# Kernel tuning notes

Hardware: AMD Instinct MI355X
Metric: run time of the kernel (lower is better)

The kernel has to match this reference:

```python
import jax, jax.numpy as jnp
import numpy as np

N_NODES = 50000


def gcn_conv(x, W, b, row, col, n):
    """PyG GCNConv with default add_self_loops=True, normalize=True.
    out[i] = sum_{e: col[e]=i} d^-1/2[row[e]] d^-1/2[i] * (x@W)[row[e]]
             + d^-1[i]*(x@W)[i] + b,  where d = in-degree + 1 (self-loop).
    """
    x_lin = x @ W                                   # [n, out_ch]
    ones = jnp.ones(row.shape[0], dtype=x.dtype)
    deg = jax.ops.segment_sum(ones, col, num_segments=n) + 1.0  # self-loop
    dinv = jax.lax.rsqrt(deg)                       # deg >= 1, safe
    norm = dinv[row] * dinv[col]                    # [E]
    msg = norm[:, None] * x_lin[row]                # [E, out_ch]
    agg = jax.ops.segment_sum(msg, col, num_segments=n)
    self_term = (dinv * dinv)[:, None] * x_lin      # self-loop contribution
    return agg + self_term + b


def setup_inputs() -> dict:
    key = jax.random.key(0)
    ks = jax.random.split(key, 10)
    in_ch, hid, out_ch = 128, 256, 64
    E = 800000
    x = jax.random.normal(ks[0], (N_NODES, in_ch), dtype=jnp.float32)
    edge_attr = jax.random.normal(ks[1], (E, 8), dtype=jnp.float32)  # unused by forward
    edge_index = jax.random.randint(ks[2], (2, E), 0, N_NODES, dtype=jnp.int64)
    def glorot(k, fan_in, fan_out):
        s = float(np.sqrt(6.0 / (fan_in + fan_out)))
        return jax.random.uniform(k, (fan_in, fan_out), jnp.float32, -s, s)
    return {
        "x": x,
        "edge_attr": edge_attr,
        "edge_index": edge_index,
        "W1": glorot(ks[3], in_ch, hid), "b1": jnp.zeros((hid,), jnp.float32),
        "W2": glorot(ks[4], hid, hid),  "b2": jnp.zeros((hid,), jnp.float32),
        "W3": glorot(ks[5], hid, out_ch), "b3": jnp.zeros((out_ch,), jnp.float32),
    }


def reference(x, edge_attr, edge_index, W1, b1, W2, b2, W3, b3):
    n = x.shape[0]
    row, col = edge_index[0], edge_index[1]
    h = jax.nn.sigmoid(gcn_conv(x, W1, b1, row, col, n))
    h = jax.nn.sigmoid(gcn_conv(h, W2, b2, row, col, n))
    # dropout(p=0.1) in eval mode is identity
    return gcn_conv(h, W3, b3, row, col, n)
```

## Files before the change

kernel.cpp:

```cpp
#include <hip/hip_runtime.h>
#include <hip/hip_bf16.h>

typedef __bf16 bf16x8_t __attribute__((ext_vector_type(8)));
typedef float f32x4_t __attribute__((ext_vector_type(4)));
typedef float f32x2_t __attribute__((ext_vector_type(2)));

__device__ __forceinline__ float bits2f(unsigned int u) {
    union { unsigned int u; float f; } c; c.u = u; return c.f;
}
__device__ __forceinline__ unsigned short f2bf_bits(float f) {
    __hip_bfloat16 h = __float2bfloat16(f);
    return __builtin_bit_cast(unsigned short, h);
}
__device__ __forceinline__ f32x2_t unpack_bf2(unsigned int u) {
    return (f32x2_t){bits2f(u << 16), bits2f(u & 0xffff0000u)};
}

__global__ void sentinel_fill(float* __restrict__ out, int n) {
    int i = blockIdx.x * blockDim.x + threadIdx.x;
    if (i < n) out[i] = 100.0f;
}

__global__ void init_combo(const unsigned int* __restrict__ ei, int* __restrict__ flags,
                           int* __restrict__ cnt, int M) {
    if (blockIdx.x == 0) {
        if (threadIdx.x < 64) {
            int lane = threadIdx.x;
            int cz = 0;
            #pragma unroll
            for (int j = 0; j < 4; ++j) {
                int idx = lane * 4 + j;
                cz += (ei[2 * idx + 1] == 0u);
            }
            #pragma unroll
            for (int off = 32; off; off >>= 1) cz += __shfl_down(cz, off);
            if (lane == 0) flags[0] = (cz > 200);
        }
    } else {
        int i = (blockIdx.x - 1) * 256 + threadIdx.x;
        if (i < M) cnt[i] = 0;
    }
}


__global__ void count_rank_dual2(const int* __restrict__ ei, int* __restrict__ cnt,
                                 int* __restrict__ rank, int* __restrict__ c32,
                                 int* __restrict__ r32, int E, int M,
                                 const int* __restrict__ flags) {
    int e = blockIdx.x * blockDim.x + threadIdx.x;
    if (e < E) {
        int r, c;
        if (flags[0]) { r = ei[2 * e]; c = ei[2 * E + 2 * e]; }
        else          { r = ei[e];     c = ei[E + e]; }
        c32[e] = c;
        r32[e] = r;
        int rk = 0;
        if ((unsigned)c < (unsigned)M) rk = atomicAdd(&cnt[c], 1);
        rank[e] = rk;
    }
}

__global__ void scan_blocks(const int* __restrict__ cnt, int* __restrict__ excl,
                            int* __restrict__ bsum, int n) {
    int tid = threadIdx.x;
    int i = blockIdx.x * 256 + tid;
    int lane = tid & 63, wv = tid >> 6;
    __shared__ int ws[4];
    int v = (i < n) ? cnt[i] : 0;
    int s = v;
    #pragma unroll
    for (int off = 1; off < 64; off <<= 1) {
        int t = __shfl_up(s, off);
        if (lane >= off) s += t;
    }
    if (lane == 63) ws[wv] = s;
    __syncthreads();
    if (tid == 0) { int a = 0; for (int q = 0; q < 4; ++q) { int t = ws[q]; ws[q] = a; a += t; } }
    __syncthreads();
    int ex = s - v + ws[wv];
    if (i < n) excl[i] = ex;
    if (tid == 255) bsum[blockIdx.x] = ex + v;
}

__global__ void scan_bsums(const int* __restrict__ bsum, int* __restrict__ boff,
                           int nb, int* __restrict__ colptr, int n) {
    int tid = threadIdx.x, lane = tid & 63, wv = tid >> 6;
    __shared__ int ws[4];
    __shared__ int carry;
    if (tid == 0) carry = 0;
    __syncthreads();
    for (int base = 0; base < nb; base += 256) {
        int i = base + tid;
        int v = (i < nb) ? bsum[i] : 0;
        int s = v;
        #pragma unroll
        for (int off = 1; off < 64; off <<= 1) {
            int t = __shfl_up(s, off);
            if (lane >= off) s += t;
        }
        if (lane == 63) ws[wv] = s;
        __syncthreads();
        if (tid == 0) { int a = carry; for (int q = 0; q < 4; ++q) { int t = ws[q]; ws[q] = a; a += t; } carry = a; }
        __syncthreads();
        int ex = s - v + ws[wv];
        if (i < nb) boff[i] = ex;
        __syncthreads();
    }
    if (tid == 0) colptr[n] = carry;
}

__global__ void scan_add_dinv(const int* __restrict__ excl, const int* __restrict__ boff,
                              const int* __restrict__ cnt, int* __restrict__ colptr,
                              float* __restrict__ dinv, int n) {
    int i = blockIdx.x * 256 + threadIdx.x;
    if (i < n) {
        colptr[i] = excl[i] + boff[blockIdx.x];
        dinv[i] = rsqrtf((float)cnt[i] + 1.0f);
    }
}

__global__ void fill_csr_part2(const int* __restrict__ c32, const int* __restrict__ r32,
                               const int* __restrict__ colptr, const int* __restrict__ rank,
                               int* __restrict__ esrc, int E, int M, int psz) {
    int part = blockIdx.x & 7;
    int e = (blockIdx.x >> 3) * 256 + threadIdx.x;
    int lo = part * psz;
    int hi = lo + psz; if (hi > M) hi = M;
    if (e < E) {
        int c = c32[e];
        if (c >= lo && c < hi) {
            int r = r32[e];
            if ((unsigned)r < (unsigned)M) {
                int p = colptr[c] + rank[e];
                if ((unsigned)p < (unsigned)E) esrc[p] = r;
            }
        }
    }
}

__global__ void prep_fused(const float* __restrict__ x, const float* __restrict__ dinv,
                           unsigned char* __restrict__ xs8,
                           const float* __restrict__ W1, const float* __restrict__ W2,
                           const float* __restrict__ W3,
                           unsigned short* __restrict__ Wt1, unsigned short* __restrict__ Wt2,
                           unsigned short* __restrict__ Wt3,
                           int M, int nps) {
    if ((int)blockIdx.x < nps) {
        int i = blockIdx.x * 256 + threadIdx.x;
        if (i < M * 32) {
            int row = i >> 5;
            float dv = dinv[row];
            float4 v = *(const float4*)(x + (size_t)i * 4);
            unsigned u = __builtin_amdgcn_cvt_pk_fp8_f32(v.x * dv, v.y * dv, 0, false);
            u = __builtin_amdgcn_cvt_pk_fp8_f32(v.z * dv, v.w * dv, u, true);
            *(unsigned*)(xs8 + (size_t)i * 4) = u;
        }
    } else {
        int i = ((int)blockIdx.x - nps) * 256 + threadIdx.x;
        if (i < 32768) {
            int k = i >> 8, n = i & 255;
            Wt1[n * 128 + k] = f2bf_bits(W1[i]);
        } else if (i < 32768 + 65536) {
            int j = i - 32768;
            int k = j >> 8, n = j & 255;
            Wt2[n * 256 + k] = f2bf_bits(W2[j]);
        } else if (i < 114688) {
            int j = i - 98304;
            int k = j >> 6, n = j & 63;
            Wt3[n * 256 + k] = f2bf_bits(W3[j]);
        }
    }
}

template<int K, int BN, int NTOT, int EPI>
__global__ __launch_bounds__(256) void gemm_tile(
    const __bf16* __restrict__ A,
    const unsigned short* __restrict__ Bt,
    const float* __restrict__ dinv,
    const float* __restrict__ bias,
    void* __restrict__ Y,
    int M)
{
    constexpr int KS = (K > 128) ? 128 : K;
    constexpr int KP = KS + 8;
    constexpr int NT = BN / 2 / 16;
    __shared__ unsigned short Bs[BN * KP];

    const int tid  = threadIdx.x;
    const int lane = tid & 63;
    const int wave = tid >> 6;
    const int wm   = wave >> 1;
    const int wn   = wave & 1;
    const int quad = lane >> 4;
    const int l16  = lane & 15;
    const int n0   = blockIdx.y * BN;

    int mrow[4];
#pragma unroll
    for (int mt = 0; mt < 4; ++mt) {
        int r = blockIdx.x * 128 + wm * 64 + mt * 16 + l16;
        mrow[mt] = (r < M) ? r : (M - 1);
    }

    f32x4_t acc[4][NT];
#pragma unroll
    for (int mt = 0; mt < 4; ++mt)
#pragma unroll
        for (int t = 0; t < NT; ++t) acc[mt][t] = (f32x4_t){0.f, 0.f, 0.f, 0.f};

    const unsigned short* BsW = &Bs[(wn * (BN / 2)) * KP];

    for (int kh = 0; kh < K; kh += KS) {
        constexpr int CH = BN * KS / 8;
        for (int idx = tid; idx < CH; idx += 256) {
            int n  = idx / (KS / 8);
            int k8 = idx - n * (KS / 8);
            uint4 v = *(const uint4*)(Bt + (size_t)(n0 + n) * K + kh + k8 * 8);
            *(uint4*)&Bs[n * KP + k8 * 8] = v;
        }
        __syncthreads();

#pragma unroll
        for (int kc = 0; kc < KS; kc += 32) {
            bf16x8_t a[4], b[NT];
#pragma unroll
            for (int mt = 0; mt < 4; ++mt)
                a[mt] = *(const bf16x8_t*)(A + (size_t)mrow[mt] * K + kh + kc + quad * 8);
#pragma unroll
            for (int t = 0; t < NT; ++t)
                b[t] = *(const bf16x8_t*)&BsW[(t * 16 + l16) * KP + kc + quad * 8];
#pragma unroll
            for (int mt = 0; mt < 4; ++mt)
#pragma unroll
                for (int t = 0; t < NT; ++t)
                    acc[mt][t] = __builtin_amdgcn_mfma_f32_16x16x32_bf16(a[mt], b[t], acc[mt][t], 0, 0, 0);
        }
        if (kh + KS < K) __syncthreads();
    }

    float bv[NT];
    if constexpr (EPI == 1) {
#pragma unroll
        for (int t = 0; t < NT; ++t)
            bv[t] = bias[n0 + wn * (BN / 2) + t * 16 + l16];
    }

#pragma unroll
    for (int mt = 0; mt < 4; ++mt) {
        int rowbase = blockIdx.x * 128 + wm * 64 + mt * 16 + quad * 4;
#pragma unroll
        for (int r = 0; r < 4; ++r) {
            int rrow = rowbase + r;
            if (rrow < M) {
                if constexpr (EPI == 0) {
                    float dv = dinv[rrow];
#pragma unroll
                    for (int t = 0; t < NT; ++t) {
                        int ccol = n0 + wn * (BN / 2) + t * 16 + l16;
                        ((__hip_bfloat16*)Y)[(size_t)rrow * NTOT + ccol] =
                            __float2bfloat16(acc[mt][t][r] * dv);
                    }
                } else if constexpr (EPI == 1) {
#pragma unroll
                    for (int t = 0; t < NT; ++t) {
                        int ccol = n0 + wn * (BN / 2) + t * 16 + l16;
                        float o = acc[mt][t][r] + bv[t];
                        o = 1.f / (1.f + __expf(-o));
                        ((__hip_bfloat16*)Y)[(size_t)rrow * NTOT + ccol] = __float2bfloat16(o);
                    }
                } else {
                    float dv = dinv[rrow];
#pragma unroll
                    for (int t = 0; t < NT; ++t) {
                        int ccol = n0 + wn * (BN / 2) + t * 16 + l16;
                        float o = acc[mt][t][r] * dv;
                        int pk = __builtin_amdgcn_cvt_pk_fp8_f32(o, o, 0, false);
                        ((unsigned char*)Y)[(size_t)rrow * NTOT + ccol] = (unsigned char)(pk & 0xff);
                    }
                }
            }
        }
    }
}

__global__ __launch_bounds__(256) void aggregate_fp8_v4(
    const unsigned char* __restrict__ Y8,
    const int* __restrict__ colptr,
    const int* __restrict__ esrc,
    const float* __restrict__ dinv,
    const float* __restrict__ bias,
    unsigned short* __restrict__ H,
    int M, int Etot)
{
    const int lane = threadIdx.x & 63;
    const int wave = threadIdx.x >> 6;
    int node = blockIdx.x * 4 + wave;
    if (node >= M) return;

    int s = colptr[node];
    int e = colptr[node + 1];
    if (s < 0) s = 0;
    if (e > Etot) e = Etot;
    if (e < s) e = s;
    int n = e - s;

    const char* Yb = (const char*)Y8;
    const unsigned lb = (unsigned)(lane * 4);

    unsigned su = *(const unsigned*)(Yb + (((unsigned)node) << 8) + lb);

    f32x2_t a0 = {0.f, 0.f}, a1 = {0.f, 0.f};

    auto gather8 = [&](unsigned* u, int base) {
        #pragma unroll
        for (int k = 0; k < 8; ++k) {
            unsigned off = (((unsigned)esrc[s + base + k]) << 8) + lb;
            u[k] = *(const unsigned*)(Yb + off);
        }
    };
    auto acc8 = [&](const unsigned* u) {
        #pragma unroll
        for (int k = 0; k < 8; ++k) {
            a0 += __builtin_amdgcn_cvt_pk_f32_fp8(u[k], false);
            a1 += __builtin_amdgcn_cvt_pk_f32_fp8(u[k], true);
        }
    };

    unsigned ua[8], ub[8];
    int NB = n >> 3;
    if (NB > 0) {
        gather8(ua, 0);
        int i = 1;
        for (; i + 1 < NB; i += 2) {
            gather8(ub, i << 3);
            acc8(ua);
            gather8(ua, (i + 1) << 3);
            acc8(ub);
        }
        if (i < NB) {
            gather8(ub, i << 3);
            acc8(ua);
            acc8(ub);
        } else {
            acc8(ua);
        }
    }
    #pragma unroll 2
    for (int t = NB << 3; t < n; ++t) {
        unsigned off = (((unsigned)esrc[s + t]) << 8) + lb;
        unsigned u = *(const unsigned*)(Yb + off);
        a0 += __builtin_amdgcn_cvt_pk_f32_fp8(u, false);
        a1 += __builtin_amdgcn_cvt_pk_f32_fp8(u, true);
    }
    a0 += __builtin_amdgcn_cvt_pk_f32_fp8(su, false);
    a1 += __builtin_amdgcn_cvt_pk_f32_fp8(su, true);

    float dv = dinv[node];
    float4 bv = *(const float4*)(bias + lane * 4);
    float o0 = a0[0] * dv + bv.x;
    float o1 = a0[1] * dv + bv.y;
    float o2 = a1[0] * dv + bv.z;
    float o3 = a1[1] * dv + bv.w;
    o0 = 1.f / (1.f + __expf(-o0));
    o1 = 1.f / (1.f + __expf(-o1));
    o2 = 1.f / (1.f + __expf(-o2));
    o3 = 1.f / (1.f + __expf(-o3));
    uint2 st;
    st.x = (unsigned)f2bf_bits(o0) | ((unsigned)f2bf_bits(o1) << 16);
    st.y = (unsigned)f2bf_bits(o2) | ((unsigned)f2bf_bits(o3) << 16);
    *(uint2*)(H + (size_t)node * 256 + lane * 4) = st;
}

__global__ __launch_bounds__(256) void aggregate_xs8b(
    const unsigned char* __restrict__ X8,
    const int* __restrict__ colptr,
    const int* __restrict__ esrc,
    const float* __restrict__ dinv,
    unsigned short* __restrict__ xa,
    int M, int Etot)
{
    const int lane = threadIdx.x & 63;
    const int wave = threadIdx.x >> 6;
    const int l4 = lane & 15;
    const int g4 = lane >> 4;
    int node = blockIdx.x * 4 + wave;
    if (node >= M) return;

    int s = colptr[node];
    int e = colptr[node + 1];
    if (s < 0) s = 0;
    if (e > Etot) e = Etot;
    if (e < s) e = s;
    int n = e - s;

    const char* Yb = (const char*)X8;
    const unsigned lb = (unsigned)(l4 * 8);

    uint2 su = {0u, 0u};
    if (g4 == 0) su = *(const uint2*)(Yb + ((unsigned)node) * 128u + lb);

    f32x2_t a0 = {0.f, 0.f}, a1 = {0.f, 0.f}, a2 = {0.f, 0.f}, a3 = {0.f, 0.f};

    auto gat = [&](uint2* u, int base) {
        u[0] = *(const uint2*)(Yb + ((unsigned)esrc[s + base + g4]) * 128u + lb);
        u[1] = *(const uint2*)(Yb + ((unsigned)esrc[s + base + 4 + g4]) * 128u + lb);
    };
    auto acc = [&](const uint2* u) {
        #pragma unroll
        for (int k = 0; k < 2; ++k) {
            a0 += __builtin_amdgcn_cvt_pk_f32_fp8(u[k].x, false);
            a1 += __builtin_amdgcn_cvt_pk_f32_fp8(u[k].x, true);
            a2 += __builtin_amdgcn_cvt_pk_f32_fp8(u[k].y, false);
            a3 += __builtin_amdgcn_cvt_pk_f32_fp8(u[k].y, true);
        }
    };

    uint2 ua[2], ub[2];
    int NB = n >> 3;
    if (NB > 0) {
        gat(ua, 0);
        int i = 1;
        for (; i + 1 < NB; i += 2) {
            gat(ub, i << 3); acc(ua);
            gat(ua, (i + 1) << 3); acc(ub);
        }
        if (i < NB) { gat(ub, i << 3); acc(ua); acc(ub); }
        else acc(ua);
    }
    for (int t = NB << 3; t < n; t += 4) {
        if (t + g4 < n) {
            uint2 u = *(const uint2*)(Yb + ((unsigned)esrc[s + t + g4]) * 128u + lb);
            a0 += __builtin_amdgcn_cvt_pk_f32_fp8(u.x, false);
            a1 += __builtin_amdgcn_cvt_pk_f32_fp8(u.x, true);
            a2 += __builtin_amdgcn_cvt_pk_f32_fp8(u.y, false);
            a3 += __builtin_amdgcn_cvt_pk_f32_fp8(u.y, true);
        }
    }
    if (g4 == 0) {
        a0 += __builtin_amdgcn_cvt_pk_f32_fp8(su.x, false);
        a1 += __builtin_amdgcn_cvt_pk_f32_fp8(su.x, true);
        a2 += __builtin_amdgcn_cvt_pk_f32_fp8(su.y, false);
        a3 += __builtin_amdgcn_cvt_pk_f32_fp8(su.y, true);
    }

    #pragma unroll
    for (int off = 16; off < 64; off <<= 1) {
        a0[0] += __shfl_xor(a0[0], off); a0[1] += __shfl_xor(a0[1], off);
        a1[0] += __shfl_xor(a1[0], off); a1[1] += __shfl_xor(a1[1], off);
        a2[0] += __shfl_xor(a2[0], off); a2[1] += __shfl_xor(a2[1], off);
        a3[0] += __shfl_xor(a3[0], off); a3[1] += __shfl_xor(a3[1], off);
    }

    if (g4 == 0) {
        float dv = dinv[node];
        uint4 st;
        st.x = (unsigned)f2bf_bits(a0[0] * dv) | ((unsigned)f2bf_bits(a0[1] * dv) << 16);
        st.y = (unsigned)f2bf_bits(a1[0] * dv) | ((unsigned)f2bf_bits(a1[1] * dv) << 16);
        st.z = (unsigned)f2bf_bits(a2[0] * dv) | ((unsigned)f2bf_bits(a2[1] * dv) << 16);
        st.w = (unsigned)f2bf_bits(a3[0] * dv) | ((unsigned)f2bf_bits(a3[1] * dv) << 16);
        *(uint4*)(xa + (size_t)node * 128 + l4 * 8) = st;
    }
}

__global__ __launch_bounds__(256) void aggregate_bf16_64_v5(
    const unsigned short* __restrict__ Yin,
    const int* __restrict__ colptr,
    const int* __restrict__ esrc,
    const float* __restrict__ dinv,
    const float* __restrict__ bias,
    float* __restrict__ out,
    int M, int Etot)
{
    const int lane = threadIdx.x & 63;
    const int wave = threadIdx.x >> 6;
    const int l4 = lane & 15;
    const int g4 = lane >> 4;
    int node = blockIdx.x * 4 + wave;
    if (node >= M) return;

    int s = colptr[node];
    int e = colptr[node + 1];
    if (s < 0) s = 0;
    if (e > Etot) e = Etot;
    if (e < s) e = s;
    int n = e - s;

    const char* Yb = (const char*)Yin;
    const unsigned lb = (unsigned)(l4 * 8);

    uint2 su = {0u, 0u};
    if (g4 == 0) su = *(const uint2*)(Yb + ((unsigned)node) * 128u + lb);

    f32x2_t a0 = {0.f, 0.f}, a1 = {0.f, 0.f};

    auto gat = [&](uint2* u, int base) {
        u[0] = *(const uint2*)(Yb + ((unsigned)esrc[s + base + g4]) * 128u + lb);
        u[1] = *(const uint2*)(Yb + ((unsigned)esrc[s + base + 4 + g4]) * 128u + lb);
    };
    auto acc = [&](const uint2* u) {
        #pragma unroll
        for (int k = 0; k < 2; ++k) {
            a0 += unpack_bf2(u[k].x);
            a1 += unpack_bf2(u[k].y);
        }
    };

    uint2 ua[2], ub[2];
    int NB = n >> 3;
    if (NB > 0) {
        gat(ua, 0);
        int i = 1;
        for (; i + 1 < NB; i += 2) {
            gat(ub, i << 3); acc(ua);
            gat(ua, (i + 1) << 3); acc(ub);
        }
        if (i < NB) { gat(ub, i << 3); acc(ua); acc(ub); }
        else acc(ua);
    }
    for (int t = NB << 3; t < n; t += 4) {
        if (t + g4 < n) {
            uint2 u = *(const uint2*)(Yb + ((unsigned)esrc[s + t + g4]) * 128u + lb);
            a0 += unpack_bf2(u.x);
            a1 += unpack_bf2(u.y);
        }
    }
    if (g4 == 0) {
        a0 += unpack_bf2(su.x);
        a1 += unpack_bf2(su.y);
    }

    #pragma unroll
    for (int off = 16; off < 64; off <<= 1) {
        a0[0] += __shfl_xor(a0[0], off); a0[1] += __shfl_xor(a0[1], off);
        a1[0] += __shfl_xor(a1[0], off); a1[1] += __shfl_xor(a1[1], off);
    }

    if (g4 == 0) {
        float dv = dinv[node];
        float4 bv = *(const float4*)(bias + l4 * 4);
        float4 st;
        st.x = a0[0] * dv + bv.x;
        st.y = a0[1] * dv + bv.y;
        st.z = a1[0] * dv + bv.z;
        st.w = a1[1] * dv + bv.w;
        *(float4*)(out + (size_t)node * 64 + l4 * 4) = st;
    }
}


extern "C" void kernel_launch(void* const* d_in, const int* in_sizes, int n_in,
                              void* d_out, int out_size, void* d_ws, size_t ws_size,
                              hipStream_t stream)
{
    int iEI = 2, iW1 = 3, iB1 = 4, iW2 = 5, iB2 = 6, iW3 = 7, iB3 = 8;
    if (n_in == 8) { iEI = 1; iW1 = 2; iB1 = 3; iW2 = 4; iB2 = 5; iW3 = 6; iB3 = 7; }

    const float* x  = (const float*)d_in[0];
    const int* ei   = (const int*)d_in[iEI];
    const float* W1 = (const float*)d_in[iW1];
    const float* b1 = (const float*)d_in[iB1];
    const float* W2 = (const float*)d_in[iW2];
    const float* b2 = (const float*)d_in[iB2];
    const float* W3 = (const float*)d_in[iW3];
    const float* b3 = (const float*)d_in[iB3];

    const int M = in_sizes[0] / 128;
    const int E = in_sizes[iEI] / 2;
    const int NB = (M + 255) / 256;
    const int PSZ = (M + 7) / 8;

    auto rnd = [](size_t b) { return (b + 255) & ~(size_t)255; };
    size_t needed = rnd(64 * 4)
                  + rnd((size_t)M * 4) * 2
                  + rnd((size_t)(M + 1) * 4)
                  + rnd((size_t)M * 4)
                  + rnd((size_t)(NB + 1) * 4) * 2
                  + rnd((size_t)E * 4) * 4
                  + rnd((size_t)256 * 128 * 2)
                  + rnd((size_t)256 * 256 * 2)
                  + rnd((size_t)64 * 256 * 2)
                  + rnd((size_t)M * 256 * 2) * 2;
    if (ws_size < needed) {
        sentinel_fill<<<(out_size + 255) / 256, 256, 0, stream>>>((float*)d_out, out_size);
        return;
    }

    char* p = (char*)d_ws;
    auto alloc = [&](size_t bytes) {
        char* r = p;
        p += (bytes + 255) & ~(size_t)255;
        return r;
    };
    int* flags  = (int*)alloc(64 * 4);
    float* dinv = (float*)alloc((size_t)M * 4);
    int* cnt    = (int*)alloc((size_t)M * 4);
    int* colptr = (int*)alloc((size_t)(M + 1) * 4);
    int* excl   = (int*)alloc((size_t)M * 4);
    int* bsum   = (int*)alloc((size_t)(NB + 1) * 4);
    int* boff   = (int*)alloc((size_t)(NB + 1) * 4);
    int* esrc   = (int*)alloc((size_t)E * 4);
    int* rank   = (int*)alloc((size_t)E * 4);
    int* c32    = (int*)alloc((size_t)E * 4);
    int* r32    = (int*)alloc((size_t)E * 4);
    unsigned short* Wt1 = (unsigned short*)alloc((size_t)256 * 128 * 2);
    unsigned short* Wt2 = (unsigned short*)alloc((size_t)256 * 256 * 2);
    unsigned short* Wt3 = (unsigned short*)alloc((size_t)64 * 256 * 2);
    __hip_bfloat16* ybuf = (__hip_bfloat16*)alloc((size_t)M * 256 * 2);
    __hip_bfloat16* hbuf = (__hip_bfloat16*)alloc((size_t)M * 256 * 2);

    unsigned char* xs8 = (unsigned char*)ybuf;
    unsigned short* xa = (unsigned short*)ybuf + (size_t)M * 128;
    unsigned char*  y8 = (unsigned char*)ybuf;

    init_combo<<<NB + 1, 256, 0, stream>>>((const unsigned int*)ei, flags, cnt, M);
    count_rank_dual2<<<(E + 255) / 256, 256, 0, stream>>>(ei, cnt, rank, c32, r32, E, M, flags);
    scan_blocks<<<NB, 256, 0, stream>>>(cnt, excl, bsum, M);
    scan_bsums<<<1, 256, 0, stream>>>(bsum, boff, NB, colptr, M);
    scan_add_dinv<<<NB, 256, 0, stream>>>(excl, boff, cnt, colptr, dinv, M);
    fill_csr_part2<<<((E + 255) / 256) * 8, 256, 0, stream>>>(
        c32, r32, colptr, rank, esrc, E, M, PSZ);

    int gmb = (M + 127) / 128;
    int ga  = (M + 3) / 4;
    int nps = (M * 32 + 255) / 256;

    prep_fused<<<nps + 448, 256, 0, stream>>>(
        x, dinv, xs8, W1, W2, W3, Wt1, Wt2, Wt3, M, nps);

    aggregate_xs8b<<<ga, 256, 0, stream>>>(
        xs8, colptr, esrc, dinv, xa, M, E);
    gemm_tile<128, 128, 256, 1><<<dim3(gmb, 2), 256, 0, stream>>>(
        (const __bf16*)xa, Wt1, dinv, b1, hbuf, M);
    gemm_tile<256, 128, 256, 2><<<dim3(gmb, 2), 256, 0, stream>>>(
        (const __bf16*)hbuf, Wt2, dinv, b2, y8, M);
    aggregate_fp8_v4<<<ga, 256, 0, stream>>>(
        y8, colptr, esrc, dinv, b2, (unsigned short*)hbuf, M, E);
    gemm_tile<256, 64, 64, 0><<<dim3(gmb, 1), 256, 0, stream>>>(
        (const __bf16*)hbuf, Wt3, dinv, b3, ybuf, M);
    aggregate_bf16_64_v5<<<ga, 256, 0, stream>>>(
        (const unsigned short*)ybuf, colptr, esrc, dinv, b3, (float*)d_out, M, E);
}
```

Measured before the change: 325.4 us.

## Privatize in-degree counters per XCD to avoid cross-die atomic traffic

The degree-counting atomics now go to one counter array per XCD, chosen by the hardware XCC_ID register, with workgroup-scope atomics. Each edge records its XCD, and the scan first builds per-XCD prefix offsets that CSR fill adds to the rank. The aim is to keep atomics in each die's local L2 instead of using device-scope atomics that have to stay coherent across dies. In exchange, counter memory grows eightfold, an extra per-edge byte array is written and read, and the scan and fill do extra reads. The code also relies on workgroup-scope atomics staying correct when every workgroup on one XCD updates the same counters.

```diff
diff --git a/kernel.cpp b/kernel.cpp
--- a/kernel.cpp
+++ b/kernel.cpp
@@ -15,6 +15,11 @@
 __device__ __forceinline__ f32x2_t unpack_bf2(unsigned int u) {
     return (f32x2_t){bits2f(u << 16), bits2f(u & 0xffff0000u)};
 }
+__device__ __forceinline__ int get_xcd() {
+    unsigned v;
+    asm volatile("s_getreg_b32 %0, hwreg(HW_REG_XCC_ID)" : "=s"(v));
+    return (int)(v & 7);
+}
 
 __global__ void sentinel_fill(float* __restrict__ out, int n) {
     int i = blockIdx.x * blockDim.x + threadIdx.x;
@@ -22,7 +27,7 @@
 }
 
 __global__ void init_combo(const unsigned int* __restrict__ ei, int* __restrict__ flags,
-                           int* __restrict__ cnt, int M) {
+                           unsigned* __restrict__ cnt8, int Mln) {
     if (blockIdx.x == 0) {
         if (threadIdx.x < 64) {
             int lane = threadIdx.x;
@@ -38,35 +43,50 @@
         }
     } else {
         int i = (blockIdx.x - 1) * 256 + threadIdx.x;
-        if (i < M) cnt[i] = 0;
-    }
-}
-
-
-__global__ void count_rank_dual2(const int* __restrict__ ei, int* __restrict__ cnt,
-                                 int* __restrict__ rank, int* __restrict__ c32,
-                                 int* __restrict__ r32, int E, int M,
-                                 const int* __restrict__ flags) {
-    int e = blockIdx.x * blockDim.x + threadIdx.x;
+        if (i < Mln) cnt8[i] = 0u;
+    }
+}
+
+__global__ void count_rank_xcd(const int* __restrict__ ei, unsigned* __restrict__ cnt8,
+                               int* __restrict__ rank, int* __restrict__ c32,
+                               int* __restrict__ r32, unsigned char* __restrict__ xcd8,
+                               int E, int M, const int* __restrict__ flags) {
+    int e = blockIdx.x * 256 + threadIdx.x;
+    int xcd = get_xcd();
     if (e < E) {
         int r, c;
         if (flags[0]) { r = ei[2 * e]; c = ei[2 * E + 2 * e]; }
         else          { r = ei[e];     c = ei[E + e]; }
         c32[e] = c;
         r32[e] = r;
+        xcd8[e] = (unsigned char)xcd;
         int rk = 0;
-        if ((unsigned)c < (unsigned)M) rk = atomicAdd(&cnt[c], 1);
+        if ((unsigned)c < (unsigned)M)
+            rk = (int)__hip_atomic_fetch_add(&cnt8[(size_t)xcd * M + c], 1u,
+                                             __ATOMIC_RELAXED, __HIP_MEMORY_SCOPE_WORKGROUP);
         rank[e] = rk;
     }
 }
 
-__global__ void scan_blocks(const int* __restrict__ cnt, int* __restrict__ excl,
-                            int* __restrict__ bsum, int n) {
+__global__ void scan_blocks_x(const unsigned* __restrict__ cnt8, unsigned* __restrict__ base8,
+                              int* __restrict__ tot, int* __restrict__ excl,
+                              int* __restrict__ bsum, int M) {
     int tid = threadIdx.x;
     int i = blockIdx.x * 256 + tid;
     int lane = tid & 63, wv = tid >> 6;
     __shared__ int ws[4];
-    int v = (i < n) ? cnt[i] : 0;
+    int v = 0;
+    if (i < M) {
+        unsigned run = 0;
+        #pragma unroll
+        for (int x = 0; x < 8; ++x) {
+            unsigned cv = cnt8[(size_t)x * M + i];
+            base8[(size_t)x * M + i] = run;
+            run += cv;
+        }
+        v = (int)run;
+        tot[i] = v;
+    }
     int s = v;
     #pragma unroll
     for (int off = 1; off < 64; off <<= 1) {
@@ -78,7 +98,7 @@
     if (tid == 0) { int a = 0; for (int q = 0; q < 4; ++q) { int t = ws[q]; ws[q] = a; a += t; } }
     __syncthreads();
     int ex = s - v + ws[wv];
-    if (i < n) excl[i] = ex;
+    if (i < M) excl[i] = ex;
     if (tid == 255) bsum[blockIdx.x] = ex + v;
 }
 
@@ -110,16 +130,18 @@
 }
 
 __global__ void scan_add_dinv(const int* __restrict__ excl, const int* __restrict__ boff,
-                              const int* __restrict__ cnt, int* __restrict__ colptr,
+                              const int* __restrict__ tot, int* __restrict__ colptr,
                               float* __restrict__ dinv, int n) {
     int i = blockIdx.x * 256 + threadIdx.x;
     if (i < n) {
         colptr[i] = excl[i] + boff[blockIdx.x];
-        dinv[i] = rsqrtf((float)cnt[i] + 1.0f);
+        dinv[i] = rsqrtf((float)tot[i] + 1.0f);
     }
 }
 
 __global__ void fill_csr_part2(const int* __restrict__ c32, const int* __restrict__ r32,
+                               const unsigned char* __restrict__ xcd8,
+                               const unsigned* __restrict__ base8,
                                const int* __restrict__ colptr, const int* __restrict__ rank,
                                int* __restrict__ esrc, int E, int M, int psz) {
     int part = blockIdx.x & 7;
@@ -131,7 +153,7 @@
         if (c >= lo && c < hi) {
             int r = r32[e];
             if ((unsigned)r < (unsigned)M) {
-                int p = colptr[c] + rank[e];
+                int p = colptr[c] + (int)base8[(size_t)xcd8[e] * M + c] + rank[e];
                 if ((unsigned)p < (unsigned)E) esrc[p] = r;
             }
         }
@@ -571,11 +593,14 @@
 
     auto rnd = [](size_t b) { return (b + 255) & ~(size_t)255; };
     size_t needed = rnd(64 * 4)
-                  + rnd((size_t)M * 4) * 2
+                  + rnd((size_t)M * 4)
+                  + rnd((size_t)M * 32) * 2
+                  + rnd((size_t)M * 4)
                   + rnd((size_t)(M + 1) * 4)
                   + rnd((size_t)M * 4)
                   + rnd((size_t)(NB + 1) * 4) * 2
                   + rnd((size_t)E * 4) * 4
+                  + rnd((size_t)E)
                   + rnd((size_t)256 * 128 * 2)
                   + rnd((size_t)256 * 256 * 2)
                   + rnd((size_t)64 * 256 * 2)
@@ -593,7 +618,9 @@
     };
     int* flags  = (int*)alloc(64 * 4);
     float* dinv = (float*)alloc((size_t)M * 4);
-    int* cnt    = (int*)alloc((size_t)M * 4);
+    unsigned* cnt8  = (unsigned*)alloc((size_t)M * 32);
+    unsigned* base8 = (unsigned*)alloc((size_t)M * 32);
+    int* tot    = (int*)alloc((size_t)M * 4);
     int* colptr = (int*)alloc((size_t)(M + 1) * 4);
     int* excl   = (int*)alloc((size_t)M * 4);
     int* bsum   = (int*)alloc((size_t)(NB + 1) * 4);
@@ -602,6 +629,7 @@
     int* rank   = (int*)alloc((size_t)E * 4);
     int* c32    = (int*)alloc((size_t)E * 4);
     int* r32    = (int*)alloc((size_t)E * 4);
+    unsigned char* xcd8 = (unsigned char*)alloc((size_t)E);
     unsigned short* Wt1 = (unsigned short*)alloc((size_t)256 * 128 * 2);
     unsigned short* Wt2 = (unsigned short*)alloc((size_t)256 * 256 * 2);
     unsigned short* Wt3 = (unsigned short*)alloc((size_t)64 * 256 * 2);
@@ -612,13 +640,17 @@
     unsigned short* xa = (unsigned short*)ybuf + (size_t)M * 128;
     unsigned char*  y8 = (unsigned char*)ybuf;
 
-    init_combo<<<NB + 1, 256, 0, stream>>>((const unsigned int*)ei, flags, cnt, M);
-    count_rank_dual2<<<(E + 255) / 256, 256, 0, stream>>>(ei, cnt, rank, c32, r32, E, M, flags);
-    scan_blocks<<<NB, 256, 0, stream>>>(cnt, excl, bsum, M);
+    int Mln = M * 8;
+    init_combo<<<(Mln + 255) / 256 + 1, 256, 0, stream>>>(
+        (const unsigned int*)ei, flags, cnt8, Mln);
+
+    count_rank_xcd<<<(E + 255) / 256, 256, 0, stream>>>(
+        ei, cnt8, rank, c32, r32, xcd8, E, M, flags);
+    scan_blocks_x<<<NB, 256, 0, stream>>>(cnt8, base8, tot, excl, bsum, M);
     scan_bsums<<<1, 256, 0, stream>>>(bsum, boff, NB, colptr, M);
-    scan_add_dinv<<<NB, 256, 0, stream>>>(excl, boff, cnt, colptr, dinv, M);
+    scan_add_dinv<<<NB, 256, 0, stream>>>(excl, boff, tot, colptr, dinv, M);
     fill_csr_part2<<<((E + 255) / 256) * 8, 256, 0, stream>>>(
-        c32, r32, colptr, rank, esrc, E, M, PSZ);
+        c32, r32, xcd8, base8, colptr, rank, esrc, E, M, PSZ);
 
     int gmb = (M + 127) / 128;
     int ga  = (M + 3) / 4;
```

Result: no change. 327.1 us (+0.5%).
